# Kernel tuning notes

Measured on AMD Instinct MI355X. Metric: run time of the kernel, lower is better.

Reference implementation:

```python
import jax, jax.numpy as jnp
import numpy as np

B, S, D, H = 8, 2048, 512, 8
NEG = -1e9


def setup_inputs() -> dict:
    key = jax.random.key(0)
    ks = jax.random.split(key, 12)
    inp = {
        "v": jax.random.normal(ks[0], (B, S, D), jnp.float32),
        "k": jax.random.normal(ks[1], (B, S, D), jnp.float32),
        "q": jax.random.normal(ks[2], (B, S, D), jnp.float32),
    }
    # pad_mask: 1.0 where key position is padding ([B,1,1,S]); random valid lengths
    lens = jax.random.randint(ks[3], (B,), S // 2, S + 1)
    inp["pad_mask"] = (jnp.arange(S)[None, :] >= lens[:, None]).astype(jnp.float32)[:, None, None, :]
    # head_mask: causal look-ahead mask, 1.0 above diagonal ([1,1,S,S])
    inp["head_mask"] = jnp.triu(jnp.ones((S, S), jnp.float32), k=1)[None, None]
    # Dense layer params (Keras Dense: y = x @ W + b)
    sc = 1.0 / np.sqrt(D)
    inp["Wq"] = jax.random.normal(ks[4], (D, D), jnp.float32) * sc
    inp["bq"] = jnp.zeros((D,), jnp.float32)
    inp["Wk"] = jax.random.normal(ks[5], (D, D), jnp.float32) * sc
    inp["bk"] = jnp.zeros((D,), jnp.float32)
    inp["Wv"] = jax.random.normal(ks[6], (D, D), jnp.float32) * sc
    inp["bv"] = jnp.zeros((D,), jnp.float32)
    inp["Wo"] = jax.random.normal(ks[7], (D, D), jnp.float32) * sc
    inp["bo"] = jnp.zeros((D,), jnp.float32)
    inp["num_heads"] = H
    return inp


def reference(v, k, q, pad_mask, head_mask, Wq, bq, Wk, bk, Wv, bv, Wo, bo, num_heads):
    b, s, d = q.shape
    depth = d // num_heads

    def split_heads(x):  # [b,s,d] -> [b,h,s,depth]
        return x.reshape(b, -1, num_heads, depth).transpose(0, 2, 1, 3)

    qh = split_heads(q @ Wq + bq)
    kh = split_heads(k @ Wk + bk)
    vh = split_heads(v @ Wv + bv)

    scale = 1.0 / jnp.sqrt(jnp.asarray(depth, qh.dtype))
    scores = jnp.einsum("bhqd,bhkd->bhqk", qh, kh) * scale
    scores = scores + pad_mask * NEG + head_mask * NEG
    attn = jax.nn.softmax(scores, axis=-1)
    ctx = jnp.einsum("bhqk,bhkd->bhqd", attn, vh)
    concat = ctx.transpose(0, 2, 1, 3).reshape(b, -1, d)
    return concat @ Wo + bo
```

## Files before the change

### kernel.cpp

```cpp
#include <hip/hip_runtime.h>

#define B_ 8
#define S_ 2048
#define D_ 512
#define H_ 8
#define HD_ 64

typedef __attribute__((ext_vector_type(8))) short short8;
typedef __attribute__((ext_vector_type(4))) short short4v;
typedef __attribute__((ext_vector_type(4))) float f32x4;
typedef __attribute__((ext_vector_type(16))) float f32x16;
typedef __attribute__((ext_vector_type(8))) __bf16 bf16x8;
typedef __attribute__((ext_vector_type(4))) unsigned uint4v;

__device__ __forceinline__ short f2bf(float f) {
    union { float f; unsigned u; } x; x.f = f;
    unsigned r = x.u + 0x7fffu + ((x.u >> 16) & 1u);
    return (short)(r >> 16);
}

__device__ __forceinline__ unsigned cvtpk(float a, float b) {
    unsigned r;
    asm("v_cvt_pk_bf16_f32 %0, %1, %2" : "=v"(r) : "v"(a), "v"(b));
    return r;
}

__device__ __forceinline__ f32x4 mfma16(short8 a, short8 b, f32x4 c) {
    return __builtin_amdgcn_mfma_f32_16x16x32_bf16(
        __builtin_bit_cast(bf16x8, a), __builtin_bit_cast(bf16x8, b), c, 0, 0, 0);
}

__device__ __forceinline__ f32x16 mfma32(short8 a, short8 b, f32x16 c) {
    return __builtin_amdgcn_mfma_f32_32x32x16_bf16(
        __builtin_bit_cast(bf16x8, a), __builtin_bit_cast(bf16x8, b), c, 0, 0, 0);
}

__device__ __forceinline__ f32x16 zero16() {
    f32x16 z;
    #pragma unroll
    for (int i = 0; i < 16; ++i) z[i] = 0.f;
    return z;
}

__global__ __launch_bounds__(256) void prep_wt(
    const float* __restrict__ W0, const float* __restrict__ W1,
    const float* __restrict__ W2, const float* __restrict__ W3,
    short* __restrict__ T0, short* __restrict__ T1,
    short* __restrict__ T2, short* __restrict__ T3)
{
    const float* W = (blockIdx.z == 0) ? W0 : (blockIdx.z == 1) ? W1 : (blockIdx.z == 2) ? W2 : W3;
    short* T = (blockIdx.z == 0) ? T0 : (blockIdx.z == 1) ? T1 : (blockIdx.z == 2) ? T2 : T3;
    __shared__ float t_s[64][65];
    const int tid = threadIdx.x;
    const int k0 = blockIdx.x * 64, n0 = blockIdx.y * 64;
    const int col = tid & 63, rg = tid >> 6;
    #pragma unroll
    for (int j = 0; j < 16; ++j) {
        const int row = rg * 16 + j;
        t_s[row][col] = W[(size_t)(k0 + row) * D_ + n0 + col];
    }
    __syncthreads();
    #pragma unroll
    for (int j = 0; j < 16; ++j) {
        const int nn = rg * 16 + j;
        T[(size_t)(n0 + nn) * D_ + k0 + col] = f2bf(t_s[col][nn]);
    }
}

__global__ __launch_bounds__(512) void qkv_gemm(
    const float* __restrict__ q_in, const float* __restrict__ k_in, const float* __restrict__ v_in,
    const short* __restrict__ wtq, const short* __restrict__ wtk, const short* __restrict__ wtv,
    const float* __restrict__ bq, const float* __restrict__ bk, const float* __restrict__ bv,
    short* __restrict__ qh, short* __restrict__ kh, short* __restrict__ vtb, float qscale)
{
    const int id = blockIdx.x;
    const int xcd = id & 7;
    const int slot = id >> 3;
    const int n0 = (slot & 3) * 128;
    const int pidx = xcd * 48 + (slot >> 2);
    const int z = pidx >> 7;
    const int m0 = (pidx & 127) * 128;

    const float* Ain = (z == 0) ? q_in : (z == 1) ? k_in : v_in;
    const short* Wt  = (z == 0) ? wtq  : (z == 1) ? wtk  : wtv;
    const float* bias = (z == 0) ? bq : (z == 1) ? bk : bv;
    short* Cout = (z == 0) ? qh : (z == 1) ? kh : vtb;
    const float osc = (z == 0) ? qscale : 1.0f;
    const int N = D_, K = D_;

    __shared__ __align__(16) short a_s[128 * 72];
    __shared__ __align__(16) short bt_s[128 * 72];

    const int tid = threadIdx.x;
    const int lane = tid & 63, wave = tid >> 6;
    const int wr = wave >> 2, wc = wave & 3;
    const int lr = lane & 15, lg = lane >> 4;

    const int srow = tid >> 3, sch = (tid & 7) * 8;

    f32x4 acc[4][2] = {};

    f32x4 fa[4];
    short8 bs[2];
    {
        const f32x4* ap0 = (const f32x4*)(Ain + (size_t)(m0 + srow) * K + sch);
        fa[0] = ap0[0]; fa[1] = ap0[1];
        const f32x4* ap1 = (const f32x4*)(Ain + (size_t)(m0 + srow + 64) * K + sch);
        fa[2] = ap1[0]; fa[3] = ap1[1];
        bs[0] = *(const short8*)(Wt + (size_t)(n0 + srow) * K + sch);
        bs[1] = *(const short8*)(Wt + (size_t)(n0 + srow + 64) * K + sch);
    }

    for (int k0 = 0; k0 < K; k0 += 64) {
        __syncthreads();
        {
            const uint4v u0 = { cvtpk(fa[0][0], fa[0][1]), cvtpk(fa[0][2], fa[0][3]),
                                cvtpk(fa[1][0], fa[1][1]), cvtpk(fa[1][2], fa[1][3]) };
            *(short8*)&a_s[srow * 72 + sch] = __builtin_bit_cast(short8, u0);
            const uint4v u1 = { cvtpk(fa[2][0], fa[2][1]), cvtpk(fa[2][2], fa[2][3]),
                                cvtpk(fa[3][0], fa[3][1]), cvtpk(fa[3][2], fa[3][3]) };
            *(short8*)&a_s[(srow + 64) * 72 + sch] = __builtin_bit_cast(short8, u1);
            *(short8*)&bt_s[srow * 72 + sch] = bs[0];
            *(short8*)&bt_s[(srow + 64) * 72 + sch] = bs[1];
        }
        __syncthreads();
        if (k0 + 64 < K) {
            const f32x4* ap0 = (const f32x4*)(Ain + (size_t)(m0 + srow) * K + k0 + 64 + sch);
            fa[0] = ap0[0]; fa[1] = ap0[1];
            const f32x4* ap1 = (const f32x4*)(Ain + (size_t)(m0 + srow + 64) * K + k0 + 64 + sch);
            fa[2] = ap1[0]; fa[3] = ap1[1];
            bs[0] = *(const short8*)(Wt + (size_t)(n0 + srow) * K + k0 + 64 + sch);
            bs[1] = *(const short8*)(Wt + (size_t)(n0 + srow + 64) * K + k0 + 64 + sch);
        }

        #pragma unroll
        for (int kc = 0; kc < 2; ++kc) {
            short8 af[4], bf[2];
            #pragma unroll
            for (int m = 0; m < 4; ++m)
                af[m] = *(const short8*)&a_s[(wr * 64 + m * 16 + lr) * 72 + kc * 32 + lg * 8];
            #pragma unroll
            for (int n = 0; n < 2; ++n)
                bf[n] = *(const short8*)&bt_s[(wc * 32 + n * 16 + lr) * 72 + kc * 32 + lg * 8];
            __builtin_amdgcn_s_setprio(1);
            #pragma unroll
            for (int m = 0; m < 4; ++m)
                #pragma unroll
                for (int n = 0; n < 2; ++n)
                    acc[m][n] = mfma16(af[m], bf[n], acc[m][n]);
            __builtin_amdgcn_s_setprio(0);
        }
    }

    float bvv[2];
    #pragma unroll
    for (int n = 0; n < 2; ++n) bvv[n] = bias[n0 + wc * 32 + n * 16 + lr];

    if (z == 2) {
        #pragma unroll
        for (int m = 0; m < 4; ++m) {
            const int row0 = m0 + wr * 64 + m * 16 + lg * 4;
            const int bb = row0 >> 11, s0 = row0 & (S_ - 1);
            #pragma unroll
            for (int n = 0; n < 2; ++n) {
                const int col = n0 + wc * 32 + n * 16 + lr;
                uint2 wv;
                wv.x = cvtpk(acc[m][n][0] + bvv[n], acc[m][n][1] + bvv[n]);
                wv.y = cvtpk(acc[m][n][2] + bvv[n], acc[m][n][3] + bvv[n]);
                *(uint2*)(Cout + ((size_t)col * B_ + bb) * S_ + s0) = wv;
            }
        }
    } else {
        #pragma unroll
        for (int m = 0; m < 4; ++m)
            #pragma unroll
            for (int i = 0; i < 4; ++i) {
                const size_t row = m0 + wr * 64 + m * 16 + lg * 4 + i;
                #pragma unroll
                for (int n = 0; n < 2; ++n) {
                    const int col = n0 + wc * 32 + n * 16 + lr;
                    Cout[row * N + col] = f2bf((acc[m][n][i] + bvv[n]) * osc);
                }
            }
    }
}

__global__ __launch_bounds__(512) void out_gemm(
    const short* __restrict__ Ain, const short* __restrict__ Wt,
    const float* __restrict__ bias, float* __restrict__ Cout)
{
    const int id = blockIdx.x;
    const int xcd = id & 7;
    const int slot = id >> 3;
    const int n0 = (slot & 3) * 128;
    const int m0 = (xcd * 16 + (slot >> 2)) * 128;
    const int N = D_, K = D_;

    __shared__ __align__(16) short a_s[128 * 72];
    __shared__ __align__(16) short bt_s[128 * 72];

    const int tid = threadIdx.x;
    const int lane = tid & 63, wave = tid >> 6;
    const int wr = wave >> 2, wc = wave & 3;
    const int lr = lane & 15, lg = lane >> 4;
    const int srow = tid >> 3, sch = (tid & 7) * 8;

    f32x4 acc[4][2] = {};

    short8 as[2], bs[2];
    {
        as[0] = *(const short8*)(Ain + (size_t)(m0 + srow) * K + sch);
        as[1] = *(const short8*)(Ain + (size_t)(m0 + srow + 64) * K + sch);
        bs[0] = *(const short8*)(Wt + (size_t)(n0 + srow) * K + sch);
        bs[1] = *(const short8*)(Wt + (size_t)(n0 + srow + 64) * K + sch);
    }

    for (int k0 = 0; k0 < K; k0 += 64) {
        __syncthreads();
        *(short8*)&a_s[srow * 72 + sch] = as[0];
        *(short8*)&a_s[(srow + 64) * 72 + sch] = as[1];
        *(short8*)&bt_s[srow * 72 + sch] = bs[0];
        *(short8*)&bt_s[(srow + 64) * 72 + sch] = bs[1];
        __syncthreads();
        if (k0 + 64 < K) {
            as[0] = *(const short8*)(Ain + (size_t)(m0 + srow) * K + k0 + 64 + sch);
            as[1] = *(const short8*)(Ain + (size_t)(m0 + srow + 64) * K + k0 + 64 + sch);
            bs[0] = *(const short8*)(Wt + (size_t)(n0 + srow) * K + k0 + 64 + sch);
            bs[1] = *(const short8*)(Wt + (size_t)(n0 + srow + 64) * K + k0 + 64 + sch);
        }

        #pragma unroll
        for (int kc = 0; kc < 2; ++kc) {
            short8 af[4], bf[2];
            #pragma unroll
            for (int m = 0; m < 4; ++m)
                af[m] = *(const short8*)&a_s[(wr * 64 + m * 16 + lr) * 72 + kc * 32 + lg * 8];
            #pragma unroll
            for (int n = 0; n < 2; ++n)
                bf[n] = *(const short8*)&bt_s[(wc * 32 + n * 16 + lr) * 72 + kc * 32 + lg * 8];
            __builtin_amdgcn_s_setprio(1);
            #pragma unroll
            for (int m = 0; m < 4; ++m)
                #pragma unroll
                for (int n = 0; n < 2; ++n)
                    acc[m][n] = mfma16(af[m], bf[n], acc[m][n]);
            __builtin_amdgcn_s_setprio(0);
        }
    }

    float bvv[2];
    #pragma unroll
    for (int n = 0; n < 2; ++n) bvv[n] = bias[n0 + wc * 32 + n * 16 + lr];
    #pragma unroll
    for (int m = 0; m < 4; ++m)
        #pragma unroll
        for (int i = 0; i < 4; ++i) {
            const size_t row = m0 + wr * 64 + m * 16 + lg * 4 + i;
            #pragma unroll
            for (int n = 0; n < 2; ++n)
                Cout[row * N + n0 + wc * 32 + n * 16 + lr] = acc[m][n][i] + bvv[n];
        }
}

__global__ __launch_bounds__(128, 3) void attn_k(
    const short* __restrict__ qh, const short* __restrict__ kh,
    const short* __restrict__ vt, const float* __restrict__ pad_mask,
    short* __restrict__ ctx)
{
    const int tid = threadIdx.x;
    const int lane = tid & 63, w = tid >> 6;
    const int l31 = lane & 31, hi = lane >> 5;
    const int id = blockIdx.x;
    const int h = id & 7;
    const int b = (id >> 3) & 7;
    const int pair = id >> 6;
    const int NT = S_ / 64;

    __shared__ __align__(16) short k_s[64 * 72];
    __shared__ __align__(16) short vt_s[64 * 68];
    __shared__ float red_s[2];

    const float* pb = pad_mask + (size_t)b * S_;
    {
        const f32x4* pv4 = (const f32x4*)pb;
        float psum = 0.f;
        #pragma unroll
        for (int j = 0; j < 4; ++j) {
            const f32x4 a = pv4[tid * 4 + j];
            psum += a[0] + a[1] + a[2] + a[3];
        }
        for (int off = 1; off < 64; off <<= 1) psum += __shfl_xor(psum, off);
        if (lane == 0) red_s[w] = psum;
    }
    __syncthreads();
    const int len = S_ - (int)(red_s[0] + red_s[1] + 0.5f);

    const int srow = tid >> 1, sc0 = (tid & 1) * 32;
    const short* kbase = kh + ((size_t)b * S_ + srow) * D_ + h * HD_ + sc0;
    const short* vbase = vt + ((size_t)(h * HD_ + srow) * B_ + b) * S_ + sc0;

    for (int half = 0; half < 2; ++half) {
        const int qt = half ? (NT - 1 - pair) : pair;
        const int q0 = qt * 64;
        const int kt_end = min(qt, (len - 1) >> 6);

        const int qrow = q0 + 2 * l31 + w;
        const short* qptr = qh + ((size_t)b * S_ + qrow) * D_ + h * HD_ + hi * 8;
        short8 qf[4];
        #pragma unroll
        for (int dd = 0; dd < 4; ++dd) qf[dd] = *(const short8*)(qptr + dd * 16);

        f32x16 accA = zero16(), accB = zero16();
        float m_r = -1e30f, l_r = 0.f;
        const int kmax = min(qrow, len - 1);

        short8 kv[4], vv[4];
        #pragma unroll
        for (int p = 0; p < 4; ++p) {
            kv[p] = ((const short8*)kbase)[p];
            vv[p] = ((const short8*)vbase)[p];
        }

        for (int kt = 0; kt <= kt_end; ++kt) {
            __syncthreads();
            #pragma unroll
            for (int p = 0; p < 4; ++p)
                *(short8*)&k_s[srow * 72 + sc0 + p * 8] = kv[p];
            #pragma unroll
            for (int p = 0; p < 4; ++p) {
                *(short4v*)&vt_s[srow * 68 + sc0 + p * 8]     = __builtin_shufflevector(vv[p], vv[p], 0, 1, 2, 3);
                *(short4v*)&vt_s[srow * 68 + sc0 + p * 8 + 4] = __builtin_shufflevector(vv[p], vv[p], 4, 5, 6, 7);
            }
            __syncthreads();
            if (kt < kt_end) {
                const short* kp = kbase + (size_t)(kt + 1) * 64 * D_;
                const short* vp = vbase + (kt + 1) * 64;
                #pragma unroll
                for (int p = 0; p < 4; ++p) {
                    kv[p] = ((const short8*)kp)[p];
                    vv[p] = ((const short8*)vp)[p];
                }
            }

            f32x16 scA = zero16(), scB = zero16();
            __builtin_amdgcn_s_setprio(1);
            #pragma unroll
            for (int dd = 0; dd < 4; ++dd) {
                const short8 kfA = *(const short8*)&k_s[l31 * 72 + dd * 16 + hi * 8];
                const short8 kfB = *(const short8*)&k_s[(32 + l31) * 72 + dd * 16 + hi * 8];
                scA = mfma32(kfA, qf[dd], scA);
                scB = mfma32(kfB, qf[dd], scB);
            }
            __builtin_amdgcn_s_setprio(0);

            const bool needmask = (kt == qt) || (kt * 64 + 63 >= len);
            if (needmask) {
                #pragma unroll
                for (int reg = 0; reg < 16; ++reg) {
                    const int koff = kt * 64 + (reg & 3) + 8 * (reg >> 2) + 4 * hi;
                    if (koff > kmax)      scA[reg] = -1e30f;
                    if (koff + 32 > kmax) scB[reg] = -1e30f;
                }
            }

            float m8[8], m4[4];
            #pragma unroll
            for (int i = 0; i < 8; ++i) m8[i] = fmaxf(fmaxf(scA[i], scA[i + 8]), fmaxf(scB[i], scB[i + 8]));
            #pragma unroll
            for (int i = 0; i < 4; ++i) m4[i] = fmaxf(m8[i], m8[i + 4]);
            float mt = fmaxf(fmaxf(m4[0], m4[1]), fmaxf(m4[2], m4[3]));
            mt = fmaxf(mt, __shfl_xor(mt, 32));
            const bool nogrow = __all(mt <= m_r);
            const float mn = nogrow ? m_r : fmaxf(m_r, mt);

            #pragma unroll
            for (int i = 0; i < 16; ++i) {
                scA[i] = __builtin_amdgcn_exp2f(scA[i] - mn);
                scB[i] = __builtin_amdgcn_exp2f(scB[i] - mn);
            }
            float s8[8], s4[4];
            #pragma unroll
            for (int i = 0; i < 8; ++i) s8[i] = (scA[i] + scA[i + 8]) + (scB[i] + scB[i + 8]);
            #pragma unroll
            for (int i = 0; i < 4; ++i) s4[i] = s8[i] + s8[i + 4];
            float rs = (s4[0] + s4[1]) + (s4[2] + s4[3]);
            rs += __shfl_xor(rs, 32);

            if (nogrow) {
                l_r += rs;
            } else {
                const float fac = __builtin_amdgcn_exp2f(m_r - mn);
                l_r = l_r * fac + rs;
                m_r = mn;
                #pragma unroll
                for (int reg = 0; reg < 16; ++reg) { accA[reg] *= fac; accB[reg] *= fac; }
            }

            unsigned pw[4][4];
            #pragma unroll
            for (int kk = 0; kk < 4; ++kk) {
                const int g = kk & 1;
                unsigned w0, w1, w2, w3;
                if (kk < 2) {
                    w0 = cvtpk(scA[8 * g + 0], scA[8 * g + 1]);
                    w1 = cvtpk(scA[8 * g + 2], scA[8 * g + 3]);
                    w2 = cvtpk(scA[8 * g + 4], scA[8 * g + 5]);
                    w3 = cvtpk(scA[8 * g + 6], scA[8 * g + 7]);
                } else {
                    w0 = cvtpk(scB[8 * g + 0], scB[8 * g + 1]);
                    w1 = cvtpk(scB[8 * g + 2], scB[8 * g + 3]);
                    w2 = cvtpk(scB[8 * g + 4], scB[8 * g + 5]);
                    w3 = cvtpk(scB[8 * g + 6], scB[8 * g + 7]);
                }
                asm("v_permlane32_swap_b32 %0, %1" : "+v"(w0), "+v"(w2));
                asm("v_permlane32_swap_b32 %0, %1" : "+v"(w1), "+v"(w3));
                pw[kk][0] = w0; pw[kk][1] = w1; pw[kk][2] = w2; pw[kk][3] = w3;
            }

            __builtin_amdgcn_s_setprio(1);
            #pragma unroll
            for (int kk = 0; kk < 4; ++kk) {
                const uint4v u = { pw[kk][0], pw[kk][1], pw[kk][2], pw[kk][3] };
                const short8 pf = __builtin_bit_cast(short8, u);
                const short4v a0 = *(const short4v*)&vt_s[l31 * 68 + kk * 16 + 8 * hi];
                const short4v a1 = *(const short4v*)&vt_s[l31 * 68 + kk * 16 + 8 * hi + 4];
                const short8 afA = __builtin_shufflevector(a0, a1, 0, 1, 2, 3, 4, 5, 6, 7);
                accA = mfma32(afA, pf, accA);
                const short4v b0 = *(const short4v*)&vt_s[(32 + l31) * 68 + kk * 16 + 8 * hi];
                const short4v b1 = *(const short4v*)&vt_s[(32 + l31) * 68 + kk * 16 + 8 * hi + 4];
                const short8 afB = __builtin_shufflevector(b0, b1, 0, 1, 2, 3, 4, 5, 6, 7);
                accB = mfma32(afB, pf, accB);
            }
            __builtin_amdgcn_s_setprio(0);
        }

        const float li = __builtin_amdgcn_rcpf(l_r);
        short* cp = ctx + ((size_t)b * S_ + qrow) * D_ + h * HD_ + 4 * hi;
        #pragma unroll
        for (int g = 0; g < 4; ++g) {
            uint2 wa;
            wa.x = cvtpk(accA[4 * g + 0] * li, accA[4 * g + 1] * li);
            wa.y = cvtpk(accA[4 * g + 2] * li, accA[4 * g + 3] * li);
            *(uint2*)(cp + 8 * g) = wa;
            uint2 wb;
            wb.x = cvtpk(accB[4 * g + 0] * li, accB[4 * g + 1] * li);
            wb.y = cvtpk(accB[4 * g + 2] * li, accB[4 * g + 3] * li);
            *(uint2*)(cp + 32 + 8 * g) = wb;
        }
    }
}

extern "C" void kernel_launch(void* const* d_in, const int* in_sizes, int n_in,
                              void* d_out, int out_size, void* d_ws, size_t ws_size,
                              hipStream_t stream)
{
    const float* v_in = (const float*)d_in[0];
    const float* k_in = (const float*)d_in[1];
    const float* q_in = (const float*)d_in[2];
    const float* pad  = (const float*)d_in[3];
    const float* Wq = (const float*)d_in[5];  const float* bq = (const float*)d_in[6];
    const float* Wk = (const float*)d_in[7];  const float* bk = (const float*)d_in[8];
    const float* Wv = (const float*)d_in[9];  const float* bv = (const float*)d_in[10];
    const float* Wo = (const float*)d_in[11]; const float* bo = (const float*)d_in[12];

    const size_t elems = (size_t)B_ * S_ * D_;
    const size_t welems = (size_t)D_ * D_;
    short* qh  = (short*)d_ws;
    short* kh  = qh + elems;
    short* vtb = kh + elems;
    short* ctx = vtb + elems;
    short* wtq = ctx + elems;
    short* wtk = wtq + welems;
    short* wtv = wtk + welems;
    short* wto = wtv + welems;

    prep_wt<<<dim3(D_ / 64, D_ / 64, 4), dim3(256), 0, stream>>>(Wq, Wk, Wv, Wo, wtq, wtk, wtv, wto);

    const float qscale = 0.125f * 1.4426950408889634f;
    qkv_gemm<<<dim3(1536), dim3(512), 0, stream>>>(
        q_in, k_in, v_in, wtq, wtk, wtv, bq, bk, bv, qh, kh, vtb, qscale);

    attn_k<<<dim3(1024), dim3(128), 0, stream>>>(qh, kh, vtb, pad, ctx);

    out_gemm<<<dim3(512), dim3(512), 0, stream>>>(ctx, wto, bo, (float*)d_out);
}
```

Baseline: 131.0 us.

## Load GEMM operands via global_load_lds into double-buffered XOR-swizzled LDS

Replaces the register-staged global-to-LDS copies of bf16 operands in the QKV and output GEMMs with direct global_load_lds transfers into double-buffered shared memory. The B operand (and A in out_gemm) is pre-swizzled in global memory: the weight transpose and the attention context write XOR-permute 8-element chunks so the unpadded 64-wide LDS rows can be read conflict-free. The aim is to cut VGPR staging, LDS store instructions and one barrier per iteration in out_gemm. The price is a coupled layout contract across kernels, and relying on the barrier to order the async LDS writes.

Result: no change. 130.4 us (median of 3 runs) (-0.5%).

```diff
diff --git a/kernel.cpp b/kernel.cpp
--- a/kernel.cpp
+++ b/kernel.cpp
@@ -23,6 +23,12 @@
     unsigned r;
     asm("v_cvt_pk_bf16_f32 %0, %1, %2" : "=v"(r) : "v"(a), "v"(b));
     return r;
+}
+
+__device__ __forceinline__ void gl16(const void* g, void* l) {
+    __builtin_amdgcn_global_load_lds(
+        (const __attribute__((address_space(1))) unsigned*)g,
+        (__attribute__((address_space(3))) unsigned*)l, 16, 0, 0);
 }
 
 __device__ __forceinline__ f32x4 mfma16(short8 a, short8 b, f32x4 c) {
@@ -63,7 +69,8 @@
     #pragma unroll
     for (int j = 0; j < 16; ++j) {
         const int nn = rg * 16 + j;
-        T[(size_t)(n0 + nn) * D_ + k0 + col] = f2bf(t_s[col][nn]);
+        const int kswz = ((((col >> 3) ^ (nn & 7)) << 3) | (col & 7));
+        T[(size_t)(n0 + nn) * D_ + k0 + kswz] = f2bf(t_s[col][nn]);
     }
 }
 
@@ -89,28 +96,29 @@
     const int N = D_, K = D_;
 
     __shared__ __align__(16) short a_s[128 * 72];
-    __shared__ __align__(16) short bt_s[128 * 72];
+    __shared__ __align__(16) short b_s[2][128 * 64];
 
     const int tid = threadIdx.x;
     const int lane = tid & 63, wave = tid >> 6;
     const int wr = wave >> 2, wc = wave & 3;
     const int lr = lane & 15, lg = lane >> 4;
-
     const int srow = tid >> 3, sch = (tid & 7) * 8;
+    const int lsw = lr & 7;
 
     f32x4 acc[4][2] = {};
 
     f32x4 fa[4];
-    short8 bs[2];
     {
         const f32x4* ap0 = (const f32x4*)(Ain + (size_t)(m0 + srow) * K + sch);
         fa[0] = ap0[0]; fa[1] = ap0[1];
         const f32x4* ap1 = (const f32x4*)(Ain + (size_t)(m0 + srow + 64) * K + sch);
         fa[2] = ap1[0]; fa[3] = ap1[1];
-        bs[0] = *(const short8*)(Wt + (size_t)(n0 + srow) * K + sch);
-        bs[1] = *(const short8*)(Wt + (size_t)(n0 + srow + 64) * K + sch);
-    }
-
+        const short* bsrc = Wt + (size_t)(n0 + wave * 8 + (lane >> 3)) * K + (lane & 7) * 8;
+        gl16(bsrc, &b_s[0][wave * 512]);
+        gl16(bsrc + (size_t)64 * K, &b_s[0][4096 + wave * 512]);
+    }
+
+    int cur = 0;
     for (int k0 = 0; k0 < K; k0 += 64) {
         __syncthreads();
         {
@@ -120,8 +128,6 @@
             const uint4v u1 = { cvtpk(fa[2][0], fa[2][1]), cvtpk(fa[2][2], fa[2][3]),
                                 cvtpk(fa[3][0], fa[3][1]), cvtpk(fa[3][2], fa[3][3]) };
             *(short8*)&a_s[(srow + 64) * 72 + sch] = __builtin_bit_cast(short8, u1);
-            *(short8*)&bt_s[srow * 72 + sch] = bs[0];
-            *(short8*)&bt_s[(srow + 64) * 72 + sch] = bs[1];
         }
         __syncthreads();
         if (k0 + 64 < K) {
@@ -129,8 +135,9 @@
             fa[0] = ap0[0]; fa[1] = ap0[1];
             const f32x4* ap1 = (const f32x4*)(Ain + (size_t)(m0 + srow + 64) * K + k0 + 64 + sch);
             fa[2] = ap1[0]; fa[3] = ap1[1];
-            bs[0] = *(const short8*)(Wt + (size_t)(n0 + srow) * K + k0 + 64 + sch);
-            bs[1] = *(const short8*)(Wt + (size_t)(n0 + srow + 64) * K + k0 + 64 + sch);
+            const short* bsrc = Wt + (size_t)(n0 + wave * 8 + (lane >> 3)) * K + k0 + 64 + (lane & 7) * 8;
+            gl16(bsrc, &b_s[cur ^ 1][wave * 512]);
+            gl16(bsrc + (size_t)64 * K, &b_s[cur ^ 1][4096 + wave * 512]);
         }
 
         #pragma unroll
@@ -141,7 +148,7 @@
                 af[m] = *(const short8*)&a_s[(wr * 64 + m * 16 + lr) * 72 + kc * 32 + lg * 8];
             #pragma unroll
             for (int n = 0; n < 2; ++n)
-                bf[n] = *(const short8*)&bt_s[(wc * 32 + n * 16 + lr) * 72 + kc * 32 + lg * 8];
+                bf[n] = *(const short8*)&b_s[cur][(wc * 32 + n * 16 + lr) * 64 + (((kc * 4 + lg) ^ lsw) << 3)];
             __builtin_amdgcn_s_setprio(1);
             #pragma unroll
             for (int m = 0; m < 4; ++m)
@@ -150,6 +157,7 @@
                     acc[m][n] = mfma16(af[m], bf[n], acc[m][n]);
             __builtin_amdgcn_s_setprio(0);
         }
+        cur ^= 1;
     }
 
     float bvv[2];
@@ -196,37 +204,36 @@
     const int m0 = (xcd * 16 + (slot >> 2)) * 128;
     const int N = D_, K = D_;
 
-    __shared__ __align__(16) short a_s[128 * 72];
-    __shared__ __align__(16) short bt_s[128 * 72];
+    __shared__ __align__(16) short a_s[2][128 * 64];
+    __shared__ __align__(16) short b_s[2][128 * 64];
 
     const int tid = threadIdx.x;
     const int lane = tid & 63, wave = tid >> 6;
     const int wr = wave >> 2, wc = wave & 3;
     const int lr = lane & 15, lg = lane >> 4;
-    const int srow = tid >> 3, sch = (tid & 7) * 8;
+    const int lsw = lr & 7;
 
     f32x4 acc[4][2] = {};
 
-    short8 as[2], bs[2];
     {
-        as[0] = *(const short8*)(Ain + (size_t)(m0 + srow) * K + sch);
-        as[1] = *(const short8*)(Ain + (size_t)(m0 + srow + 64) * K + sch);
-        bs[0] = *(const short8*)(Wt + (size_t)(n0 + srow) * K + sch);
-        bs[1] = *(const short8*)(Wt + (size_t)(n0 + srow + 64) * K + sch);
-    }
-
+        const short* asrc = Ain + (size_t)(m0 + wave * 8 + (lane >> 3)) * K + (lane & 7) * 8;
+        gl16(asrc, &a_s[0][wave * 512]);
+        gl16(asrc + (size_t)64 * K, &a_s[0][4096 + wave * 512]);
+        const short* bsrc = Wt + (size_t)(n0 + wave * 8 + (lane >> 3)) * K + (lane & 7) * 8;
+        gl16(bsrc, &b_s[0][wave * 512]);
+        gl16(bsrc + (size_t)64 * K, &b_s[0][4096 + wave * 512]);
+    }
+
+    int cur = 0;
     for (int k0 = 0; k0 < K; k0 += 64) {
         __syncthreads();
-        *(short8*)&a_s[srow * 72 + sch] = as[0];
-        *(short8*)&a_s[(srow + 64) * 72 + sch] = as[1];
-        *(short8*)&bt_s[srow * 72 + sch] = bs[0];
-        *(short8*)&bt_s[(srow + 64) * 72 + sch] = bs[1];
-        __syncthreads();
         if (k0 + 64 < K) {
-            as[0] = *(const short8*)(Ain + (size_t)(m0 + srow) * K + k0 + 64 + sch);
-            as[1] = *(const short8*)(Ain + (size_t)(m0 + srow + 64) * K + k0 + 64 + sch);
-            bs[0] = *(const short8*)(Wt + (size_t)(n0 + srow) * K + k0 + 64 + sch);
-            bs[1] = *(const short8*)(Wt + (size_t)(n0 + srow + 64) * K + k0 + 64 + sch);
+            const short* asrc = Ain + (size_t)(m0 + wave * 8 + (lane >> 3)) * K + k0 + 64 + (lane & 7) * 8;
+            gl16(asrc, &a_s[cur ^ 1][wave * 512]);
+            gl16(asrc + (size_t)64 * K, &a_s[cur ^ 1][4096 + wave * 512]);
+            const short* bsrc = Wt + (size_t)(n0 + wave * 8 + (lane >> 3)) * K + k0 + 64 + (lane & 7) * 8;
+            gl16(bsrc, &b_s[cur ^ 1][wave * 512]);
+            gl16(bsrc + (size_t)64 * K, &b_s[cur ^ 1][4096 + wave * 512]);
         }
 
         #pragma unroll
@@ -234,10 +241,10 @@
             short8 af[4], bf[2];
             #pragma unroll
             for (int m = 0; m < 4; ++m)
-                af[m] = *(const short8*)&a_s[(wr * 64 + m * 16 + lr) * 72 + kc * 32 + lg * 8];
+                af[m] = *(const short8*)&a_s[cur][(wr * 64 + m * 16 + lr) * 64 + (((kc * 4 + lg) ^ lsw) << 3)];
             #pragma unroll
             for (int n = 0; n < 2; ++n)
-                bf[n] = *(const short8*)&bt_s[(wc * 32 + n * 16 + lr) * 72 + kc * 32 + lg * 8];
+                bf[n] = *(const short8*)&b_s[cur][(wc * 32 + n * 16 + lr) * 64 + (((kc * 4 + lg) ^ lsw) << 3)];
             __builtin_amdgcn_s_setprio(1);
             #pragma unroll
             for (int m = 0; m < 4; ++m)
@@ -246,6 +253,7 @@
                     acc[m][n] = mfma16(af[m], bf[n], acc[m][n]);
             __builtin_amdgcn_s_setprio(0);
         }
+        cur ^= 1;
     }
 
     float bvv[2];
@@ -435,17 +443,18 @@
         }
 
         const float li = __builtin_amdgcn_rcpf(l_r);
-        short* cp = ctx + ((size_t)b * S_ + qrow) * D_ + h * HD_ + 4 * hi;
+        const int rsw = qrow & 7;
+        short* cpb = ctx + ((size_t)b * S_ + qrow) * D_ + h * HD_ + 4 * hi;
         #pragma unroll
         for (int g = 0; g < 4; ++g) {
             uint2 wa;
             wa.x = cvtpk(accA[4 * g + 0] * li, accA[4 * g + 1] * li);
             wa.y = cvtpk(accA[4 * g + 2] * li, accA[4 * g + 3] * li);
-            *(uint2*)(cp + 8 * g) = wa;
+            *(uint2*)(cpb + ((g ^ rsw) << 3)) = wa;
             uint2 wb;
             wb.x = cvtpk(accB[4 * g + 0] * li, accB[4 * g + 1] * li);
             wb.y = cvtpk(accB[4 * g + 2] * li, accB[4 * g + 3] * li);
-            *(uint2*)(cp + 32 + 8 * g) = wb;
+            *(uint2*)(cpb + (((g + 4) ^ rsw) << 3)) = wb;
         }
     }
 }
```
